# Kernel optimization log

Hardware: AMD Instinct MI355X
Metric: run time of the kernel (lower is better)

The kernel has to match this reference:

```python
import jax, jax.numpy as jnp
import numpy as np
from jax.scipy.special import erf

ALPHA = 0.84
SSIM_WIN = 11       # monai SSIMLoss default win_size
SIGMA = 1.5         # both kernels use sigma=1.5
K1, K2, DATA_RANGE = 0.01, 0.03, 1.0


def _erf_gauss_1d(sigma=SIGMA, truncated=4.0):
    # monai.networks.layers.gaussian_1d, approx='erf', normalize=False
    tail = int(max(sigma * truncated, 0.5) + 0.5)  # 6 -> 13 taps
    x = jnp.arange(-tail, tail + 1, dtype=jnp.float32)
    t = 0.70710678 / sigma
    out = 0.5 * (erf(t * (x + 0.5)) - erf(t * (x - 0.5)))
    return jnp.clip(out, 0.0)


def _ssim_gauss_1d(win=SSIM_WIN, sigma=SIGMA):
    # monai SSIM gaussian kernel: exp-based, normalized
    d = jnp.arange(-(win - 1) / 2.0, (win + 1) / 2.0, dtype=jnp.float32)
    g = jnp.exp(-(d ** 2) / (2.0 * sigma ** 2))
    return g / g.sum()


def _conv1d(x, k, axis, pad):
    # depthwise 1D conv along spatial axis of NCHW tensor (C=1)
    ks = k.shape[0]
    if axis == 2:
        kern = k.reshape(1, 1, ks, 1)
        p = [(pad, pad), (0, 0)]
    else:
        kern = k.reshape(1, 1, 1, ks)
        p = [(0, 0), (pad, pad)]
    return jax.lax.conv_general_dilated(
        x, kern, window_strides=(1, 1), padding=p,
        dimension_numbers=('NCHW', 'OIHW', 'NCHW'))


def _sep_filter(x, k, pad):
    return _conv1d(_conv1d(x, k, 2, pad), k, 3, pad)


def setup_inputs() -> dict:
    key = jax.random.key(0)
    kx, ky = jax.random.split(key)
    shape = (64, 1, 512, 512)
    x = jax.random.uniform(kx, shape, dtype=jnp.float32)
    y = jax.random.uniform(ky, shape, dtype=jnp.float32)
    return {"x": x, "y": y}


def reference(x, y):
    kw = _ssim_gauss_1d()
    filt = lambda t: _sep_filter(t, kw, 0)
    c1 = (K1 * DATA_RANGE) ** 2
    c2 = (K2 * DATA_RANGE) ** 2
    mx, my = filt(x), filt(y)
    mxx, myy, mxy = filt(x * x), filt(y * y), filt(x * y)
    vx = mxx - mx * mx
    vy = myy - my * my
    cov = mxy - mx * my
    ssim = ((2.0 * mx * my + c1) * (2.0 * cov + c2)) / (
        (mx * mx + my * my + c1) * (vx + vy + c2))
    ssim_loss = 1.0 - jnp.mean(ssim)  # scalar, reduction='mean'

    # --- L1 branch: SAME zero-padded erf-gaussian filtering, no reduction ---
    ke = _erf_gauss_1d()
    pad = (ke.shape[0] - 1) // 2
    l1 = jnp.abs(_sep_filter(y, ke, pad) - _sep_filter(x, ke, pad))  # [N,1,H,W]

    return 100.0 * (ALPHA * ssim_loss + (1.0 - ALPHA) * l1)
```

## Files before the change

### kernel.cpp

```cpp
#include <hip/hip_runtime.h>
#include <cmath>

#define IMG_W 512
#define IMG_H 512
#define NIMG 64
#define OWV 502

struct KTaps {
    float kw[11];
    float ke[13];
};

#define WAVE_FENCE() __builtin_amdgcn_wave_barrier()

__global__ __launch_bounds__(256) void ssim_band_kernel(
        const float* __restrict__ x, const float* __restrict__ y,
        double* __restrict__ ssum, KTaps kt) {
    __shared__ __align__(16) float sq[4][2][4][80];

    const int img   = blockIdx.z;
    const int band  = blockIdx.y;
    const int strip = blockIdx.x;
    const int tid   = threadIdx.x;
    const int w     = tid >> 6;
    const int lane  = tid & 63;
    const int r0    = band * 64;
    const int wc0   = strip * 256 + w * 64;

    const float* __restrict__ xi = x + (size_t)img * IMG_H * IMG_W;
    const float* __restrict__ yi = y + (size_t)img * IMG_H * IMG_W;

    const bool stg = (lane < 38);
    const int  gc  = wc0 + 2 * lane;
    const bool gok = stg && (gc < IMG_W);

    auto ld2 = [&](const float* __restrict__ p, int r) -> float2 {
        float2 v = make_float2(0.f, 0.f);
        if (gok && r < IMG_H) v = *(const float2*)(p + (size_t)r * IMG_W + gc);
        return v;
    };

    auto stage = [&](int buf, float2 vx, float2 vy) {
        if (stg) {
            const float s0 = vx.x + vy.x, d0 = vx.x - vy.x;
            const float s1 = vx.y + vy.y, d1 = vx.y - vy.y;
            *(float2*)&sq[w][buf][0][2 * lane] = vx;
            *(float2*)&sq[w][buf][1][2 * lane] = vy;
            *(float2*)&sq[w][buf][2][2 * lane] = make_float2(s0 * s0, s1 * s1);
            *(float2*)&sq[w][buf][3][2 * lane] = make_float2(d0 * d0, d1 * d1);
        }
    };

    float acc[11][4];
#pragma unroll
    for (int i = 0; i < 11; ++i)
#pragma unroll
        for (int q = 0; q < 4; ++q) acc[i][q] = 0.f;
    float tsum = 0.f;
    const int outc = wc0 + lane;

    stage(0, ld2(xi, r0), ld2(yi, r0));
    float2 pfx[2], pfy[2];
    pfx[1] = ld2(xi, r0 + 1); pfy[1] = ld2(yi, r0 + 1);
    pfx[0] = ld2(xi, r0 + 2); pfy[0] = ld2(yi, r0 + 2);
    WAVE_FENCE();

#pragma unroll 1
    for (int c2 = 0; c2 < 4; ++c2) {
        const int rbase = c2 * 22;
#pragma unroll
        for (int p22 = 0; p22 < 22; ++p22) {
            const int rr  = rbase + p22;
            const int p11 = p22 % 11;
            const int b   = p22 & 1;
            if (rr <= 73) {
                float h[4];
#pragma unroll
                for (int q = 0; q < 4; ++q) {
                    float a0 = 0.f;
#pragma unroll
                    for (int u = 0; u < 11; ++u)
                        a0 += kt.kw[u] * sq[w][b][q][lane + u];
                    h[q] = a0;
                }
                if (rr < 73) stage(b ^ 1, pfx[(p22 + 1) & 1], pfy[(p22 + 1) & 1]);
                if (rr < 71) {
                    pfx[(p22 + 1) & 1] = ld2(xi, r0 + rr + 3);
                    pfy[(p22 + 1) & 1] = ld2(yi, r0 + rr + 3);
                }
#pragma unroll
                for (int d = 0; d <= 10; ++d) {
                    const int s = (p11 + 11 - d) % 11;
                    const float wv = kt.kw[d];
                    acc[s][0] += wv * h[0]; acc[s][1] += wv * h[1];
                    acc[s][2] += wv * h[2]; acc[s][3] += wv * h[3];
                }
                {
                    const int sc = (p11 + 1) % 11;
                    const int ro = rr - 10;
                    if (ro >= 0) {
                        const int o = r0 + ro;
                        if (o < OWV && outc < OWV) {
                            const float mx = acc[sc][0], my = acc[sc][1];
                            const float Aq = acc[sc][2], Bq = acc[sc][3];
                            const float mq   = mx * mx + my * my;
                            const float pxy  = mx * my;
                            const float vsum = 0.5f  * (Aq + Bq) - mq;
                            const float cov  = 0.25f * (Aq - Bq) - pxy;
                            const float c1 = 1e-4f, c2c = 9e-4f;
                            const float num = (2.f * pxy + c1) * (2.f * cov + c2c);
                            const float den = (mq + c1) * (vsum + c2c);
                            tsum += num * __builtin_amdgcn_rcpf(den);
                        }
                    }
#pragma unroll
                    for (int q = 0; q < 4; ++q) acc[sc][q] = 0.f;
                }
                WAVE_FENCE();
            }
        }
    }

#pragma unroll
    for (int off = 32; off > 0; off >>= 1) tsum += __shfl_down(tsum, off, 64);
    __shared__ float wsum[4];
    if (lane == 0) wsum[w] = tsum;
    __syncthreads();
    if (tid == 0) atomicAdd(ssum, (double)(wsum[0] + wsum[1] + wsum[2] + wsum[3]));
}

__global__ __launch_bounds__(256, 8) void l1_band_kernel(
        const float* __restrict__ x, const float* __restrict__ y,
        const double* __restrict__ ssum, float* __restrict__ out, KTaps kt) {
    __shared__ __align__(16) float sdw[4][2][80];

    const int img   = blockIdx.y;
    const int bx    = blockIdx.x;
    const int strip = bx & 1;
    const int band  = bx >> 1;
    const int tid   = threadIdx.x;
    const int w     = tid >> 6;
    const int lane  = tid & 63;
    const int o0    = band * 32;
    const int rin0  = o0 - 6;
    const int wc0   = strip * 256 + w * 64;

    const float* __restrict__ xi = x + (size_t)img * IMG_H * IMG_W;
    const float* __restrict__ yi = y + (size_t)img * IMG_H * IMG_W;
    float* __restrict__ oi = out + (size_t)img * IMG_H * IMG_W;

    const float base = 100.f * 0.84f * (1.f - (float)(*ssum) * (1.f / 16128256.f));

    const bool stg = (lane < 38);
    const int  gc  = wc0 - 6 + 2 * lane;
    const bool gok = stg && (gc >= 0) && (gc < IMG_W);

    auto ld2 = [&](const float* __restrict__ p, int r) -> float2 {
        float2 v = make_float2(0.f, 0.f);
        if (gok && r >= 0 && r < IMG_H) v = *(const float2*)(p + (size_t)r * IMG_W + gc);
        return v;
    };
    auto stage = [&](int buf, float2 vx, float2 vy) {
        if (stg) *(float2*)&sdw[w][buf][2 * lane] =
            make_float2(vy.x - vx.x, vy.y - vx.y);
    };

    float acc[13];
#pragma unroll
    for (int i = 0; i < 13; ++i) acc[i] = 0.f;

    stage(0, ld2(xi, rin0), ld2(yi, rin0));
    float2 pfx[2], pfy[2];
    pfx[1] = ld2(xi, rin0 + 1); pfy[1] = ld2(yi, rin0 + 1);
    pfx[0] = ld2(xi, rin0 + 2); pfy[0] = ld2(yi, rin0 + 2);
    WAVE_FENCE();

#pragma unroll 1
    for (int c2 = 0; c2 < 2; ++c2) {
        const int rbase = c2 * 26;
#pragma unroll
        for (int p26 = 0; p26 < 26; ++p26) {
            const int rr  = rbase + p26;
            const int p13 = p26 % 13;
            const int b   = p26 & 1;
            if (rr <= 43) {
                float a0 = 0.f;
#pragma unroll
                for (int u = 0; u < 13; ++u)
                    a0 += kt.ke[u] * sdw[w][b][lane + u];
                if (rr < 43) stage(b ^ 1, pfx[(p26 + 1) & 1], pfy[(p26 + 1) & 1]);
                if (rr < 41) {
                    pfx[(p26 + 1) & 1] = ld2(xi, rin0 + rr + 3);
                    pfy[(p26 + 1) & 1] = ld2(yi, rin0 + rr + 3);
                }
#pragma unroll
                for (int d = 0; d <= 12; ++d)
                    acc[(p13 + 13 - d) % 13] += kt.ke[d] * a0;
                {
                    const int sc = (p13 + 1) % 13;
                    const int ro = rr - 12;
                    if (ro >= 0) {
                        const int o = o0 + ro;
                        oi[(size_t)o * IMG_W + wc0 + lane] =
                            fmaf(16.f, fabsf(acc[sc]), base);
                    }
                    acc[sc] = 0.f;
                }
                WAVE_FENCE();
            }
        }
    }
}

extern "C" void kernel_launch(void* const* d_in, const int* in_sizes, int n_in,
                              void* d_out, int out_size, void* d_ws, size_t ws_size,
                              hipStream_t stream) {
    const float* x = (const float*)d_in[0];
    const float* y = (const float*)d_in[1];
    float* out = (float*)d_out;
    double* ssum = (double*)d_ws;

    KTaps kt;
    {
        double g[11], s = 0.0;
        for (int i = 0; i < 11; ++i) {
            const double d = (double)i - 5.0;
            g[i] = std::exp(-(d * d) / 4.5);
            s += g[i];
        }
        for (int i = 0; i < 11; ++i) kt.kw[i] = (float)(g[i] / s);
    }
    {
        const double t = 0.70710678 / 1.5;
        for (int i = 0; i < 13; ++i) {
            const double xx = (double)i - 6.0;
            const double v = 0.5 * (std::erf(t * (xx + 0.5)) - std::erf(t * (xx - 0.5)));
            kt.ke[i] = (float)(v < 0.0 ? 0.0 : v);
        }
    }

    hipMemsetAsync(ssum, 0, sizeof(double), stream);

    ssim_band_kernel<<<dim3(2, 8, NIMG), dim3(256), 0, stream>>>(x, y, ssum, kt);
    l1_band_kernel<<<dim3(32, NIMG, 1), dim3(256), 0, stream>>>(x, y, ssum, out, kt);
}
```

Before: 288.0 us.

## Use fp16 dot2 horizontal filtering and packed fp32 vertical accumulation in both kernels

Intermediate rows are staged in LDS as fp16 pairs, and the horizontal Gaussian pass uses fdot2 with per-lane shifted weight vectors. The SSIM kernel now filters sum and difference terms (x+y, x-y and their squares) instead of x, y, sum² and diff², and the vertical pass accumulates into packed float2 registers. The L1 kernel has each thread handle two output columns, so each wave covers 128 columns and the grid is halved. It also writes float2 stores and fuses the x/y difference into the load. The aim is fewer LDS bytes and fewer ALU instructions, at the cost of fp16 rounding error in the filtered values and in the SSIM statistics.

Result: faster. 269.6 us (-6.4%).

```diff
diff --git a/kernel.cpp b/kernel.cpp
--- a/kernel.cpp
+++ b/kernel.cpp
@@ -6,6 +6,10 @@
 #define NIMG 64
 #define OWV 502
 
+typedef _Float16 h2 __attribute__((ext_vector_type(2)));
+typedef _Float16 h4 __attribute__((ext_vector_type(4)));
+typedef float    f2v __attribute__((ext_vector_type(2)));
+
 struct KTaps {
     float kw[11];
     float ke[13];
@@ -13,10 +17,26 @@
 
 #define WAVE_FENCE() __builtin_amdgcn_wave_barrier()
 
+#if defined(__has_builtin)
+#if __has_builtin(__builtin_amdgcn_fdot2)
+#define FDOT2(a, b, c) __builtin_amdgcn_fdot2((a), (b), (c), false)
+#endif
+#endif
+#ifndef FDOT2
+static __device__ __forceinline__ float fdot2_sw(h2 a, h2 b, float c) {
+    return c + (float)a.x * (float)b.x + (float)a.y * (float)b.y;
+}
+#define FDOT2(a, b, c) fdot2_sw((a), (b), (c))
+#endif
+
+static __device__ __forceinline__ h2 lo2(h4 v) { return __builtin_shufflevector(v, v, 0, 1); }
+static __device__ __forceinline__ h2 hi2(h4 v) { return __builtin_shufflevector(v, v, 2, 3); }
+
 __global__ __launch_bounds__(256) void ssim_band_kernel(
         const float* __restrict__ x, const float* __restrict__ y,
         double* __restrict__ ssum, KTaps kt) {
-    __shared__ __align__(16) float sq[4][2][4][80];
+    __shared__ __align__(16) h2 pS[4][2][40], pD[4][2][40],
+                               pP[4][2][40], pQ[4][2][40];
 
     const int img   = blockIdx.z;
     const int band  = blockIdx.y;
@@ -44,18 +64,33 @@
         if (stg) {
             const float s0 = vx.x + vy.x, d0 = vx.x - vy.x;
             const float s1 = vx.y + vy.y, d1 = vx.y - vy.y;
-            *(float2*)&sq[w][buf][0][2 * lane] = vx;
-            *(float2*)&sq[w][buf][1][2 * lane] = vy;
-            *(float2*)&sq[w][buf][2][2 * lane] = make_float2(s0 * s0, s1 * s1);
-            *(float2*)&sq[w][buf][3][2 * lane] = make_float2(d0 * d0, d1 * d1);
+            h2 a; a.x = (_Float16)s0;        a.y = (_Float16)s1;        pS[w][buf][lane] = a;
+            h2 b; b.x = (_Float16)d0;        b.y = (_Float16)d1;        pD[w][buf][lane] = b;
+            h2 c; c.x = (_Float16)(s0 * s0); c.y = (_Float16)(s1 * s1); pP[w][buf][lane] = c;
+            h2 d; d.x = (_Float16)(d0 * d0); d.y = (_Float16)(d1 * d1); pQ[w][buf][lane] = d;
         }
     };
 
-    float acc[11][4];
-#pragma unroll
-    for (int i = 0; i < 11; ++i)
-#pragma unroll
-        for (int q = 0; q < 4; ++q) acc[i][q] = 0.f;
+    const int off = lane & 3;
+    h2 w2[8];
+#pragma unroll
+    for (int t = 0; t < 8; ++t) { w2[t].x = (_Float16)0.f; w2[t].y = (_Float16)0.f; }
+#pragma unroll
+    for (int offc = 0; offc < 4; ++offc) {
+        if (off == offc) {
+#pragma unroll
+            for (int u = 0; u < 11; ++u) {
+                const int j = u + offc;
+                if (j & 1) w2[j >> 1].y = (_Float16)kt.kw[u];
+                else       w2[j >> 1].x = (_Float16)kt.kw[u];
+            }
+        }
+    }
+    const int hb = 2 * (lane >> 2);
+
+    f2v acc01[11], acc23[11];
+#pragma unroll
+    for (int i = 0; i < 11; ++i) { acc01[i] = (f2v)0.f; acc23[i] = (f2v)0.f; }
     float tsum = 0.f;
     const int outc = wc0 + lane;
 
@@ -74,26 +109,31 @@
             const int p11 = p22 % 11;
             const int b   = p22 & 1;
             if (rr <= 73) {
-                float h[4];
-#pragma unroll
-                for (int q = 0; q < 4; ++q) {
-                    float a0 = 0.f;
-#pragma unroll
-                    for (int u = 0; u < 11; ++u)
-                        a0 += kt.kw[u] * sq[w][b][q][lane + u];
-                    h[q] = a0;
+                float hS = 0.f, hD = 0.f, hP = 0.f, hQ = 0.f;
+#pragma unroll
+                for (int k = 0; k < 4; ++k) {
+                    const h4 vS = *(const h4*)&pS[w][b][hb + 2 * k];
+                    const h4 vD = *(const h4*)&pD[w][b][hb + 2 * k];
+                    const h4 vP = *(const h4*)&pP[w][b][hb + 2 * k];
+                    const h4 vQ = *(const h4*)&pQ[w][b][hb + 2 * k];
+                    hS = FDOT2(w2[2 * k], lo2(vS), hS); hS = FDOT2(w2[2 * k + 1], hi2(vS), hS);
+                    hD = FDOT2(w2[2 * k], lo2(vD), hD); hD = FDOT2(w2[2 * k + 1], hi2(vD), hD);
+                    hP = FDOT2(w2[2 * k], lo2(vP), hP); hP = FDOT2(w2[2 * k + 1], hi2(vP), hP);
+                    hQ = FDOT2(w2[2 * k], lo2(vQ), hQ); hQ = FDOT2(w2[2 * k + 1], hi2(vQ), hQ);
                 }
                 if (rr < 73) stage(b ^ 1, pfx[(p22 + 1) & 1], pfy[(p22 + 1) & 1]);
                 if (rr < 71) {
                     pfx[(p22 + 1) & 1] = ld2(xi, r0 + rr + 3);
                     pfy[(p22 + 1) & 1] = ld2(yi, r0 + rr + 3);
                 }
+                f2v h01; h01.x = hS; h01.y = hD;
+                f2v h23; h23.x = hP; h23.y = hQ;
 #pragma unroll
                 for (int d = 0; d <= 10; ++d) {
                     const int s = (p11 + 11 - d) % 11;
-                    const float wv = kt.kw[d];
-                    acc[s][0] += wv * h[0]; acc[s][1] += wv * h[1];
-                    acc[s][2] += wv * h[2]; acc[s][3] += wv * h[3];
+                    f2v wv; wv.x = kt.kw[d]; wv.y = kt.kw[d];
+                    acc01[s] += wv * h01;
+                    acc23[s] += wv * h23;
                 }
                 {
                     const int sc = (p11 + 1) % 11;
@@ -101,20 +141,20 @@
                     if (ro >= 0) {
                         const int o = r0 + ro;
                         if (o < OWV && outc < OWV) {
-                            const float mx = acc[sc][0], my = acc[sc][1];
-                            const float Aq = acc[sc][2], Bq = acc[sc][3];
-                            const float mq   = mx * mx + my * my;
-                            const float pxy  = mx * my;
-                            const float vsum = 0.5f  * (Aq + Bq) - mq;
-                            const float cov  = 0.25f * (Aq - Bq) - pxy;
+                            const float S = acc01[sc].x, D = acc01[sc].y;
+                            const float P = acc23[sc].x, Q = acc23[sc].y;
+                            const float S2 = S * S, D2 = D * D;
+                            const float mq2  = 0.5f * (S2 + D2);
+                            const float px2  = 0.5f * (S2 - D2);
+                            const float vsum = 0.5f * (P + Q) - mq2;
+                            const float cov2 = 0.5f * (P - Q) - px2;
                             const float c1 = 1e-4f, c2c = 9e-4f;
-                            const float num = (2.f * pxy + c1) * (2.f * cov + c2c);
-                            const float den = (mq + c1) * (vsum + c2c);
+                            const float num = (px2 + c1) * (cov2 + c2c);
+                            const float den = (mq2 + c1) * (vsum + c2c);
                             tsum += num * __builtin_amdgcn_rcpf(den);
                         }
                     }
-#pragma unroll
-                    for (int q = 0; q < 4; ++q) acc[sc][q] = 0.f;
+                    acc01[sc] = (f2v)0.f; acc23[sc] = (f2v)0.f;
                 }
                 WAVE_FENCE();
             }
@@ -122,28 +162,26 @@
     }
 
 #pragma unroll
-    for (int off = 32; off > 0; off >>= 1) tsum += __shfl_down(tsum, off, 64);
+    for (int offr = 32; offr > 0; offr >>= 1) tsum += __shfl_down(tsum, offr, 64);
     __shared__ float wsum[4];
     if (lane == 0) wsum[w] = tsum;
     __syncthreads();
     if (tid == 0) atomicAdd(ssum, (double)(wsum[0] + wsum[1] + wsum[2] + wsum[3]));
 }
 
-__global__ __launch_bounds__(256, 8) void l1_band_kernel(
+__global__ __launch_bounds__(256) void l1_band_kernel(
         const float* __restrict__ x, const float* __restrict__ y,
         const double* __restrict__ ssum, float* __restrict__ out, KTaps kt) {
-    __shared__ __align__(16) float sdw[4][2][80];
-
-    const int img   = blockIdx.y;
-    const int bx    = blockIdx.x;
-    const int strip = bx & 1;
-    const int band  = bx >> 1;
-    const int tid   = threadIdx.x;
-    const int w     = tid >> 6;
-    const int lane  = tid & 63;
-    const int o0    = band * 32;
-    const int rin0  = o0 - 6;
-    const int wc0   = strip * 256 + w * 64;
+    __shared__ __align__(16) h2 sdw[4][2][72];
+
+    const int img  = blockIdx.y;
+    const int band = blockIdx.x;
+    const int tid  = threadIdx.x;
+    const int w    = tid >> 6;
+    const int lane = tid & 63;
+    const int o0   = band * 32;
+    const int rin0 = o0 - 6;
+    const int wc0  = w * 128;
 
     const float* __restrict__ xi = x + (size_t)img * IMG_H * IMG_W;
     const float* __restrict__ yi = y + (size_t)img * IMG_H * IMG_W;
@@ -151,28 +189,61 @@
 
     const float base = 100.f * 0.84f * (1.f - (float)(*ssum) * (1.f / 16128256.f));
 
-    const bool stg = (lane < 38);
-    const int  gc  = wc0 - 6 + 2 * lane;
-    const bool gok = stg && (gc >= 0) && (gc < IMG_W);
-
-    auto ld2 = [&](const float* __restrict__ p, int r) -> float2 {
+    const int  g0  = wc0 - 6 + 2 * lane;
+    const bool ok0 = (g0 >= 0) && (g0 < IMG_W);
+    const bool on1 = (lane >= 58);
+    const int  g1  = wc0 + 6 + 2 * lane;
+    const bool ok1 = on1 && (g1 < IMG_W);
+
+    auto ldd = [&](int r, bool ok, int g) -> float2 {
         float2 v = make_float2(0.f, 0.f);
-        if (gok && r >= 0 && r < IMG_H) v = *(const float2*)(p + (size_t)r * IMG_W + gc);
+        if (ok && r >= 0 && r < IMG_H) {
+            const float2 a  = *(const float2*)(xi + (size_t)r * IMG_W + g);
+            const float2 bb = *(const float2*)(yi + (size_t)r * IMG_W + g);
+            v = make_float2(bb.x - a.x, bb.y - a.y);
+        }
         return v;
     };
-    auto stage = [&](int buf, float2 vx, float2 vy) {
-        if (stg) *(float2*)&sdw[w][buf][2 * lane] =
-            make_float2(vy.x - vx.x, vy.y - vx.y);
+    auto stage = [&](int buf, float2 v0, float2 v1) {
+        h2 a; a.x = (_Float16)v0.x; a.y = (_Float16)v0.y;
+        sdw[w][buf][lane] = a;
+        if (on1) {
+            h2 b; b.x = (_Float16)v1.x; b.y = (_Float16)v1.y;
+            sdw[w][buf][64 + (lane - 58)] = b;
+        }
     };
 
-    float acc[13];
-#pragma unroll
-    for (int i = 0; i < 13; ++i) acc[i] = 0.f;
-
-    stage(0, ld2(xi, rin0), ld2(yi, rin0));
-    float2 pfx[2], pfy[2];
-    pfx[1] = ld2(xi, rin0 + 1); pfy[1] = ld2(yi, rin0 + 1);
-    pfx[0] = ld2(xi, rin0 + 2); pfy[0] = ld2(yi, rin0 + 2);
+    const int off = 2 * (lane & 1);
+    h2 wA[8], wB[8];
+#pragma unroll
+    for (int t = 0; t < 8; ++t) {
+        wA[t].x = (_Float16)0.f; wA[t].y = (_Float16)0.f;
+        wB[t].x = (_Float16)0.f; wB[t].y = (_Float16)0.f;
+    }
+#pragma unroll
+    for (int offc = 0; offc <= 2; offc += 2) {
+        if (off == offc) {
+#pragma unroll
+            for (int u = 0; u < 13; ++u) {
+                const int ja = u + offc;
+                if (ja & 1) wA[ja >> 1].y = (_Float16)kt.ke[u];
+                else        wA[ja >> 1].x = (_Float16)kt.ke[u];
+                const int jb = u + offc + 1;
+                if (jb & 1) wB[jb >> 1].y = (_Float16)kt.ke[u];
+                else        wB[jb >> 1].x = (_Float16)kt.ke[u];
+            }
+        }
+    }
+    const int hb = lane & ~1;
+
+    f2v acc[13];
+#pragma unroll
+    for (int i = 0; i < 13; ++i) acc[i] = (f2v)0.f;
+
+    stage(0, ldd(rin0, ok0, g0), ldd(rin0, ok1, g1));
+    float2 pf0[2], pf1[2];
+    pf0[1] = ldd(rin0 + 1, ok0, g0); pf1[1] = ldd(rin0 + 1, ok1, g1);
+    pf0[0] = ldd(rin0 + 2, ok0, g0); pf1[0] = ldd(rin0 + 2, ok1, g1);
     WAVE_FENCE();
 
 #pragma unroll 1
@@ -184,27 +255,37 @@
             const int p13 = p26 % 13;
             const int b   = p26 & 1;
             if (rr <= 43) {
-                float a0 = 0.f;
-#pragma unroll
-                for (int u = 0; u < 13; ++u)
-                    a0 += kt.ke[u] * sdw[w][b][lane + u];
-                if (rr < 43) stage(b ^ 1, pfx[(p26 + 1) & 1], pfy[(p26 + 1) & 1]);
+                float a0 = 0.f, a1 = 0.f;
+#pragma unroll
+                for (int k = 0; k < 4; ++k) {
+                    const h4 v = *(const h4*)&sdw[w][b][hb + 2 * k];
+                    const h2 vl = lo2(v), vh = hi2(v);
+                    a0 = FDOT2(wA[2 * k], vl, a0); a0 = FDOT2(wA[2 * k + 1], vh, a0);
+                    a1 = FDOT2(wB[2 * k], vl, a1); a1 = FDOT2(wB[2 * k + 1], vh, a1);
+                }
+                if (rr < 43) stage(b ^ 1, pf0[(p26 + 1) & 1], pf1[(p26 + 1) & 1]);
                 if (rr < 41) {
-                    pfx[(p26 + 1) & 1] = ld2(xi, rin0 + rr + 3);
-                    pfy[(p26 + 1) & 1] = ld2(yi, rin0 + rr + 3);
-                }
-#pragma unroll
-                for (int d = 0; d <= 12; ++d)
-                    acc[(p13 + 13 - d) % 13] += kt.ke[d] * a0;
+                    pf0[(p26 + 1) & 1] = ldd(rin0 + rr + 3, ok0, g0);
+                    pf1[(p26 + 1) & 1] = ldd(rin0 + rr + 3, ok1, g1);
+                }
+                f2v hv; hv.x = a0; hv.y = a1;
+#pragma unroll
+                for (int d = 0; d <= 12; ++d) {
+                    const int s = (p13 + 13 - d) % 13;
+                    f2v wv; wv.x = kt.ke[d]; wv.y = kt.ke[d];
+                    acc[s] += wv * hv;
+                }
                 {
                     const int sc = (p13 + 1) % 13;
                     const int ro = rr - 12;
                     if (ro >= 0) {
                         const int o = o0 + ro;
-                        oi[(size_t)o * IMG_W + wc0 + lane] =
-                            fmaf(16.f, fabsf(acc[sc]), base);
+                        f2v r;
+                        r.x = fmaf(16.f, fabsf(acc[sc].x), base);
+                        r.y = fmaf(16.f, fabsf(acc[sc].y), base);
+                        *(f2v*)&oi[(size_t)o * IMG_W + wc0 + 2 * lane] = r;
                     }
-                    acc[sc] = 0.f;
+                    acc[sc] = (f2v)0.f;
                 }
                 WAVE_FENCE();
             }
@@ -242,5 +323,5 @@
     hipMemsetAsync(ssum, 0, sizeof(double), stream);
 
     ssim_band_kernel<<<dim3(2, 8, NIMG), dim3(256), 0, stream>>>(x, y, ssum, kt);
-    l1_band_kernel<<<dim3(32, NIMG, 1), dim3(256), 0, stream>>>(x, y, ssum, out, kt);
+    l1_band_kernel<<<dim3(16, NIMG, 1), dim3(256), 0, stream>>>(x, y, ssum, out, kt);
 }
```

## Use packed fp16 dot products for SSIM and L1 separable filters

Applied to the files above, without the earlier changes.

Staging buffers move to fp16 and the horizontal and vertical Gaussian taps use packed fdot2. The SSIM vertical pass replaces its rolling accumulator array with an fp16 history ring convolved through host-precomputed rotated weights. SSIM now works on sum/difference statistics, so x and y means come from S and D. Band height is halved to give more blocks, and the L1 kernel fuses the x/y subtraction at load time. Doing the conv in fp16 cuts LDS traffic and VALU work but loses precision in the squared terms and the variance, which may hurt SSIM accuracy.

Result: faster. 271.2 us (-5.8%).

```diff
diff --git a/kernel.cpp b/kernel.cpp
--- a/kernel.cpp
+++ b/kernel.cpp
@@ -6,17 +6,40 @@
 #define NIMG 64
 #define OWV 502
 
+typedef _Float16 h2 __attribute__((ext_vector_type(2)));
+typedef _Float16 h4 __attribute__((ext_vector_type(4)));
+typedef _Float16 h8 __attribute__((ext_vector_type(8)));
+
 struct KTaps {
     float kw[11];
     float ke[13];
+    unsigned wpk[11][6];
 };
 
 #define WAVE_FENCE() __builtin_amdgcn_wave_barrier()
+
+#if defined(__has_builtin)
+#if __has_builtin(__builtin_amdgcn_fdot2)
+#define FDOT2(a, b, c) __builtin_amdgcn_fdot2((a), (b), (c), false)
+#endif
+#endif
+#ifndef FDOT2
+static __device__ __forceinline__ float fdot2_sw(h2 a, h2 b, float c) {
+    return c + (float)a.x * (float)b.x + (float)a.y * (float)b.y;
+}
+#define FDOT2(a, b, c) fdot2_sw((a), (b), (c))
+#endif
+
+static __device__ __forceinline__ h2 lo2(h4 v) { return __builtin_shufflevector(v, v, 0, 1); }
+static __device__ __forceinline__ h2 hi2(h4 v) { return __builtin_shufflevector(v, v, 2, 3); }
+static __device__ __forceinline__ h2 upk(unsigned u) {
+    union { unsigned u; h2 h; } c; c.u = u; return c.h;
+}
 
 __global__ __launch_bounds__(256) void ssim_band_kernel(
         const float* __restrict__ x, const float* __restrict__ y,
         double* __restrict__ ssum, KTaps kt) {
-    __shared__ __align__(16) float sq[4][2][4][80];
+    __shared__ __align__(16) h2 plq[4][2][40][4];
 
     const int img   = blockIdx.z;
     const int band  = blockIdx.y;
@@ -24,7 +47,7 @@
     const int tid   = threadIdx.x;
     const int w     = tid >> 6;
     const int lane  = tid & 63;
-    const int r0    = band * 64;
+    const int r0    = band * 32;
     const int wc0   = strip * 256 + w * 64;
 
     const float* __restrict__ xi = x + (size_t)img * IMG_H * IMG_W;
@@ -44,18 +67,41 @@
         if (stg) {
             const float s0 = vx.x + vy.x, d0 = vx.x - vy.x;
             const float s1 = vx.y + vy.y, d1 = vx.y - vy.y;
-            *(float2*)&sq[w][buf][0][2 * lane] = vx;
-            *(float2*)&sq[w][buf][1][2 * lane] = vy;
-            *(float2*)&sq[w][buf][2][2 * lane] = make_float2(s0 * s0, s1 * s1);
-            *(float2*)&sq[w][buf][3][2 * lane] = make_float2(d0 * d0, d1 * d1);
+            h8 st;
+            st[0] = (_Float16)s0;        st[1] = (_Float16)s1;
+            st[2] = (_Float16)d0;        st[3] = (_Float16)d1;
+            st[4] = (_Float16)(s0 * s0); st[5] = (_Float16)(s1 * s1);
+            st[6] = (_Float16)(d0 * d0); st[7] = (_Float16)(d1 * d1);
+            *(h8*)&plq[w][buf][lane][0] = st;
         }
     };
 
-    float acc[11][4];
-#pragma unroll
-    for (int i = 0; i < 11; ++i)
-#pragma unroll
-        for (int q = 0; q < 4; ++q) acc[i][q] = 0.f;
+    h2 w6[6];
+#pragma unroll
+    for (int t = 0; t < 6; ++t) { w6[t].x = (_Float16)0.f; w6[t].y = (_Float16)0.f; }
+    if (lane & 1) {
+#pragma unroll
+        for (int u = 0; u < 11; ++u) {
+            const int j = u + 1;
+            if (j & 1) w6[j >> 1].y = (_Float16)kt.kw[u];
+            else       w6[j >> 1].x = (_Float16)kt.kw[u];
+        }
+    } else {
+#pragma unroll
+        for (int u = 0; u < 11; ++u) {
+            if (u & 1) w6[u >> 1].y = (_Float16)kt.kw[u];
+            else       w6[u >> 1].x = (_Float16)kt.kw[u];
+        }
+    }
+    const int H = lane >> 1;
+
+    h2 histS[6], histD[6], histP[6], histQ[6];
+#pragma unroll
+    for (int t = 0; t < 6; ++t) {
+        histS[t].x = (_Float16)0.f; histS[t].y = (_Float16)0.f;
+        histD[t] = histS[t]; histP[t] = histS[t]; histQ[t] = histS[t];
+    }
+
     float tsum = 0.f;
     const int outc = wc0 + lane;
 
@@ -66,55 +112,62 @@
     WAVE_FENCE();
 
 #pragma unroll 1
-    for (int c2 = 0; c2 < 4; ++c2) {
+    for (int c2 = 0; c2 < 2; ++c2) {
         const int rbase = c2 * 22;
 #pragma unroll
         for (int p22 = 0; p22 < 22; ++p22) {
             const int rr  = rbase + p22;
             const int p11 = p22 % 11;
             const int b   = p22 & 1;
-            if (rr <= 73) {
-                float h[4];
-#pragma unroll
-                for (int q = 0; q < 4; ++q) {
-                    float a0 = 0.f;
-#pragma unroll
-                    for (int u = 0; u < 11; ++u)
-                        a0 += kt.kw[u] * sq[w][b][q][lane + u];
-                    h[q] = a0;
-                }
-                if (rr < 73) stage(b ^ 1, pfx[(p22 + 1) & 1], pfy[(p22 + 1) & 1]);
-                if (rr < 71) {
+            if (rr <= 41) {
+                float hS = 0.f, hD = 0.f, hP = 0.f, hQ = 0.f;
+#pragma unroll
+                for (int i = 0; i < 6; ++i) {
+                    const h8 v = *(const h8*)&plq[w][b][H + i][0];
+                    const h2 sp = __builtin_shufflevector(v, v, 0, 1);
+                    const h2 dp = __builtin_shufflevector(v, v, 2, 3);
+                    const h2 pp = __builtin_shufflevector(v, v, 4, 5);
+                    const h2 qp = __builtin_shufflevector(v, v, 6, 7);
+                    hS = FDOT2(w6[i], sp, hS);
+                    hD = FDOT2(w6[i], dp, hD);
+                    hP = FDOT2(w6[i], pp, hP);
+                    hQ = FDOT2(w6[i], qp, hQ);
+                }
+                if (p11 & 1) {
+                    histS[p11 >> 1].y = (_Float16)hS; histD[p11 >> 1].y = (_Float16)hD;
+                    histP[p11 >> 1].y = (_Float16)hP; histQ[p11 >> 1].y = (_Float16)hQ;
+                } else {
+                    histS[p11 >> 1].x = (_Float16)hS; histD[p11 >> 1].x = (_Float16)hD;
+                    histP[p11 >> 1].x = (_Float16)hP; histQ[p11 >> 1].x = (_Float16)hQ;
+                }
+                if (rr < 41) stage(b ^ 1, pfx[(p22 + 1) & 1], pfy[(p22 + 1) & 1]);
+                if (rr < 39) {
                     pfx[(p22 + 1) & 1] = ld2(xi, r0 + rr + 3);
                     pfy[(p22 + 1) & 1] = ld2(yi, r0 + rr + 3);
                 }
-#pragma unroll
-                for (int d = 0; d <= 10; ++d) {
-                    const int s = (p11 + 11 - d) % 11;
-                    const float wv = kt.kw[d];
-                    acc[s][0] += wv * h[0]; acc[s][1] += wv * h[1];
-                    acc[s][2] += wv * h[2]; acc[s][3] += wv * h[3];
-                }
                 {
-                    const int sc = (p11 + 1) % 11;
                     const int ro = rr - 10;
                     if (ro >= 0) {
+                        float S = 0.f, D = 0.f, P = 0.f, Q = 0.f;
+#pragma unroll
+                        for (int m = 0; m < 6; ++m) {
+                            const h2 wr = upk(kt.wpk[p11][m]);
+                            S = FDOT2(wr, histS[m], S); D = FDOT2(wr, histD[m], D);
+                            P = FDOT2(wr, histP[m], P); Q = FDOT2(wr, histQ[m], Q);
+                        }
                         const int o = r0 + ro;
                         if (o < OWV && outc < OWV) {
-                            const float mx = acc[sc][0], my = acc[sc][1];
-                            const float Aq = acc[sc][2], Bq = acc[sc][3];
-                            const float mq   = mx * mx + my * my;
-                            const float pxy  = mx * my;
-                            const float vsum = 0.5f  * (Aq + Bq) - mq;
-                            const float cov  = 0.25f * (Aq - Bq) - pxy;
+                            const float S2 = S * S, D2 = D * D;
+                            const float mq2  = 0.5f * (S2 + D2);
+                            const float px2  = 0.5f * (S2 - D2);
+                            const float vsum = 0.5f * (P + Q) - mq2;
+                            const float cov2 = 0.5f * (P - Q) - px2;
                             const float c1 = 1e-4f, c2c = 9e-4f;
-                            const float num = (2.f * pxy + c1) * (2.f * cov + c2c);
-                            const float den = (mq + c1) * (vsum + c2c);
+                            const float num = (px2 + c1) * (cov2 + c2c);
+                            const float den = (mq2 + c1) * (vsum + c2c);
                             tsum += num * __builtin_amdgcn_rcpf(den);
                         }
                     }
-#pragma unroll
-                    for (int q = 0; q < 4; ++q) acc[sc][q] = 0.f;
                 }
                 WAVE_FENCE();
             }
@@ -122,22 +175,21 @@
     }
 
 #pragma unroll
-    for (int off = 32; off > 0; off >>= 1) tsum += __shfl_down(tsum, off, 64);
+    for (int offr = 32; offr > 0; offr >>= 1) tsum += __shfl_down(tsum, offr, 64);
     __shared__ float wsum[4];
     if (lane == 0) wsum[w] = tsum;
     __syncthreads();
     if (tid == 0) atomicAdd(ssum, (double)(wsum[0] + wsum[1] + wsum[2] + wsum[3]));
 }
 
-__global__ __launch_bounds__(256, 8) void l1_band_kernel(
+__global__ __launch_bounds__(256) void l1_band_kernel(
         const float* __restrict__ x, const float* __restrict__ y,
         const double* __restrict__ ssum, float* __restrict__ out, KTaps kt) {
-    __shared__ __align__(16) float sdw[4][2][80];
-
-    const int img   = blockIdx.y;
-    const int bx    = blockIdx.x;
-    const int strip = bx & 1;
-    const int band  = bx >> 1;
+    __shared__ __align__(16) h2 sdw[4][2][40];
+
+    const int img   = blockIdx.z;
+    const int band  = blockIdx.y;
+    const int strip = blockIdx.x;
     const int tid   = threadIdx.x;
     const int w     = tid >> 6;
     const int lane  = tid & 63;
@@ -155,24 +207,47 @@
     const int  gc  = wc0 - 6 + 2 * lane;
     const bool gok = stg && (gc >= 0) && (gc < IMG_W);
 
-    auto ld2 = [&](const float* __restrict__ p, int r) -> float2 {
+    auto ldp = [&](int r) -> float2 {
         float2 v = make_float2(0.f, 0.f);
-        if (gok && r >= 0 && r < IMG_H) v = *(const float2*)(p + (size_t)r * IMG_W + gc);
+        if (gok && r >= 0 && r < IMG_H) {
+            const float2 a  = *(const float2*)(xi + (size_t)r * IMG_W + gc);
+            const float2 bb = *(const float2*)(yi + (size_t)r * IMG_W + gc);
+            v = make_float2(bb.x - a.x, bb.y - a.y);
+        }
         return v;
     };
-    auto stage = [&](int buf, float2 vx, float2 vy) {
-        if (stg) *(float2*)&sdw[w][buf][2 * lane] =
-            make_float2(vy.x - vx.x, vy.y - vx.y);
+    auto stage = [&](int buf, float2 v) {
+        if (stg) {
+            h2 a; a.x = (_Float16)v.x; a.y = (_Float16)v.y;
+            sdw[w][buf][lane] = a;
+        }
     };
 
+    const int off = lane & 3;
+    h2 w2[8];
+#pragma unroll
+    for (int t = 0; t < 8; ++t) { w2[t].x = (_Float16)0.f; w2[t].y = (_Float16)0.f; }
+#pragma unroll
+    for (int offc = 0; offc < 4; ++offc) {
+        if (off == offc) {
+#pragma unroll
+            for (int u = 0; u < 13; ++u) {
+                const int j = u + offc;
+                if (j & 1) w2[j >> 1].y = (_Float16)kt.ke[u];
+                else       w2[j >> 1].x = (_Float16)kt.ke[u];
+            }
+        }
+    }
+    const int bh = 2 * (lane >> 2);
+
     float acc[13];
 #pragma unroll
     for (int i = 0; i < 13; ++i) acc[i] = 0.f;
 
-    stage(0, ld2(xi, rin0), ld2(yi, rin0));
-    float2 pfx[2], pfy[2];
-    pfx[1] = ld2(xi, rin0 + 1); pfy[1] = ld2(yi, rin0 + 1);
-    pfx[0] = ld2(xi, rin0 + 2); pfy[0] = ld2(yi, rin0 + 2);
+    stage(0, ldp(rin0));
+    float2 pf[2];
+    pf[1] = ldp(rin0 + 1);
+    pf[0] = ldp(rin0 + 2);
     WAVE_FENCE();
 
 #pragma unroll 1
@@ -186,13 +261,13 @@
             if (rr <= 43) {
                 float a0 = 0.f;
 #pragma unroll
-                for (int u = 0; u < 13; ++u)
-                    a0 += kt.ke[u] * sdw[w][b][lane + u];
-                if (rr < 43) stage(b ^ 1, pfx[(p26 + 1) & 1], pfy[(p26 + 1) & 1]);
-                if (rr < 41) {
-                    pfx[(p26 + 1) & 1] = ld2(xi, rin0 + rr + 3);
-                    pfy[(p26 + 1) & 1] = ld2(yi, rin0 + rr + 3);
-                }
+                for (int k = 0; k < 4; ++k) {
+                    const h4 v = *(const h4*)&sdw[w][b][bh + 2 * k];
+                    a0 = FDOT2(w2[2 * k], lo2(v), a0);
+                    a0 = FDOT2(w2[2 * k + 1], hi2(v), a0);
+                }
+                if (rr < 43) stage(b ^ 1, pf[(p26 + 1) & 1]);
+                if (rr < 41) pf[(p26 + 1) & 1] = ldp(rin0 + rr + 3);
 #pragma unroll
                 for (int d = 0; d <= 12; ++d)
                     acc[(p13 + 13 - d) % 13] += kt.ke[d] * a0;
@@ -212,6 +287,20 @@
     }
 }
 
+static unsigned short f32_to_f16_bits(float f) {
+    union { float f; unsigned u; } v; v.f = f;
+    const unsigned u = v.u;
+    const unsigned s = (u >> 16) & 0x8000u;
+    int e = (int)((u >> 23) & 0xff) - 127 + 15;
+    unsigned m = u & 0x7fffffu;
+    if (e <= 0) return (unsigned short)s;
+    if (e >= 31) return (unsigned short)(s | 0x7c00u);
+    unsigned h = s | ((unsigned)e << 10) | (m >> 13);
+    const unsigned rem = m & 0x1fffu;
+    if (rem > 0x1000u || (rem == 0x1000u && (h & 1u))) h++;
+    return (unsigned short)h;
+}
+
 extern "C" void kernel_launch(void* const* d_in, const int* in_sizes, int n_in,
                               void* d_out, int out_size, void* d_ws, size_t ws_size,
                               hipStream_t stream) {
@@ -221,6 +310,7 @@
     double* ssum = (double*)d_ws;
 
     KTaps kt;
+    float kwf[11];
     {
         double g[11], s = 0.0;
         for (int i = 0; i < 11; ++i) {
@@ -228,7 +318,7 @@
             g[i] = std::exp(-(d * d) / 4.5);
             s += g[i];
         }
-        for (int i = 0; i < 11; ++i) kt.kw[i] = (float)(g[i] / s);
+        for (int i = 0; i < 11; ++i) { kwf[i] = (float)(g[i] / s); kt.kw[i] = kwf[i]; }
     }
     {
         const double t = 0.70710678 / 1.5;
@@ -238,9 +328,24 @@
             kt.ke[i] = (float)(v < 0.0 ? 0.0 : v);
         }
     }
+    {
+        for (int p = 0; p < 11; ++p) {
+            for (int m = 0; m < 6; ++m) {
+                const int s0 = 2 * m, s1 = 2 * m + 1;
+                const int d0 = ((s0 - p - 1) % 11 + 11) % 11;
+                unsigned lo = f32_to_f16_bits(kwf[d0]);
+                unsigned hi = 0;
+                if (s1 <= 10) {
+                    const int d1 = ((s1 - p - 1) % 11 + 11) % 11;
+                    hi = f32_to_f16_bits(kwf[d1]);
+                }
+                kt.wpk[p][m] = lo | (hi << 16);
+            }
+        }
+    }
 
     hipMemsetAsync(ssum, 0, sizeof(double), stream);
 
-    ssim_band_kernel<<<dim3(2, 8, NIMG), dim3(256), 0, stream>>>(x, y, ssum, kt);
-    l1_band_kernel<<<dim3(32, NIMG, 1), dim3(256), 0, stream>>>(x, y, ssum, out, kt);
-}
+    ssim_band_kernel<<<dim3(2, 16, NIMG), dim3(256), 0, stream>>>(x, y, ssum, kt);
+    l1_band_kernel<<<dim3(2, 16, NIMG), dim3(256), 0, stream>>>(x, y, ssum, out, kt);
+}
```
